# Performance work log

Measured on AMD Instinct MI355X. Metric: run time of the kernel, lower is better.

Reference implementation:

```python
import jax, jax.numpy as jnp
import numpy as np


def setup_inputs() -> dict:
    key = jax.random.key(0)
    k1, k2 = jax.random.split(key)
    embeddings = jax.random.normal(k1, (32, 512, 1024), dtype=jnp.float32)
    aspect = jax.random.normal(k2, (32, 1024), dtype=jnp.float32)
    return {"embeddings": embeddings, "aspect": aspect}


def reference(embeddings, aspect):
    # go_backwards=False, so no sequence reversal.
    # L2-normalize embeddings per token and aspect per sample.
    e = embeddings / jnp.linalg.norm(embeddings, axis=2, keepdims=True)
    a = aspect / jnp.linalg.norm(aspect, axis=1, keepdims=True)
    # NaN-mask (zero-norm rows produce NaN after division).
    e = jnp.where(jnp.isnan(e), jnp.zeros_like(e), e)
    a = jnp.where(jnp.isnan(a), jnp.zeros_like(a), a)
    # Circulant matrix: circ[b, i, j] = a[b, (j - i) mod D]
    # (matches the TF scatter_nd construction M[i, (i+k)%D] = a[k]).
    D = e.shape[-1]
    r = jnp.arange(D)
    idx = (r[None, :] - r[:, None]) % D  # [D, D]
    circ = a[:, idx]  # [B, D, D]
    # matmul(e, circ, transpose_b=True): out[b,s,i] = sum_j e[b,s,j] * circ[b,i,j]
    return jnp.einsum('bsd,bid->bsi', e, circ)
```

## Files before the change

kernel.cpp:

```cpp
#include <hip/hip_runtime.h>
#include <hip/hip_bf16.h>

typedef __attribute__((ext_vector_type(8))) short bf16x8;
typedef __attribute__((ext_vector_type(4))) float f32x4;

#define NB 32
#define NS 512
#define ND 1024

__device__ __forceinline__ unsigned short f2bf(float f) {
  unsigned int u = __float_as_uint(f);
  u = (u + 0x7FFFu + ((u >> 16) & 1u)) >> 16;
  return (unsigned short)u;
}

__global__ void anorm_kernel(const float* __restrict__ aspect,
                             unsigned short* __restrict__ a_n) {
  int b = blockIdx.x;
  int t = threadIdx.x;
  const float4* p = (const float4*)(aspect + (size_t)b * ND);
  float4 v = p[t];
  float s = v.x * v.x + v.y * v.y + v.z * v.z + v.w * v.w;
#pragma unroll
  for (int off = 32; off >= 1; off >>= 1) s += __shfl_down(s, off);
  __shared__ float red[4];
  if ((t & 63) == 0) red[t >> 6] = s;
  __syncthreads();
  float tot = red[0] + red[1] + red[2] + red[3];
  float inv = (tot > 0.f) ? (1.f / sqrtf(tot)) : 0.f;
  ushort4 u;
  u.x = f2bf(v.x * inv); u.y = f2bf(v.y * inv);
  u.z = f2bf(v.z * inv); u.w = f2bf(v.w * inv);
  ((ushort4*)(a_n + (size_t)b * ND))[t] = u;
}

__global__ __launch_bounds__(256)
void enormbf_kernel(const float* __restrict__ emb,
                    unsigned short* __restrict__ eN) {
  int wave = threadIdx.x >> 6, lane = threadIdx.x & 63;
  size_t row = (size_t)blockIdx.x * 4 + wave;
  const float4* p = (const float4*)(emb + row * ND);
  float4 v[4];
  float s = 0.f;
#pragma unroll
  for (int j = 0; j < 4; ++j) {
    v[j] = p[lane + 64 * j];
    s += v[j].x * v[j].x + v[j].y * v[j].y + v[j].z * v[j].z + v[j].w * v[j].w;
  }
#pragma unroll
  for (int off = 32; off >= 1; off >>= 1) s += __shfl_xor(s, off);
  float inv = (s > 0.f) ? (1.f / sqrtf(s)) : 0.f;
  ushort4* o = (ushort4*)(eN + row * ND);
#pragma unroll
  for (int j = 0; j < 4; ++j) {
    ushort4 u;
    u.x = f2bf(v[j].x * inv); u.y = f2bf(v[j].y * inv);
    u.z = f2bf(v[j].z * inv); u.w = f2bf(v[j].w * inv);
    o[lane + 64 * j] = u;
  }
}

__global__ __launch_bounds__(256, 4)
void corr_gemm3_kernel(const unsigned short* __restrict__ eN,
                       const unsigned short* __restrict__ a_n,
                       float* __restrict__ out) {
  __shared__ unsigned short copies[8][1160];
  __shared__ unsigned short Atile[128 * 64];

  const int b = blockIdx.x, mt = blockIdx.y, nt = blockIdx.z;
  const int n0 = nt * 128, m0 = mt * 128;
  const int t = threadIdx.x;

  {
    const unsigned short* an = a_n + (size_t)b * ND;
    int p = t & 7;
    int x0 = (t >> 3) * 36;
    int base = (896 - n0 + p) & 1023;
#pragma unroll
    for (int j = 0; j < 36; j += 4) {
      ushort4 u;
      u.x = an[(base + x0 + j + 0) & 1023];
      u.y = an[(base + x0 + j + 1) & 1023];
      u.z = an[(base + x0 + j + 2) & 1023];
      u.w = an[(base + x0 + j + 3) & 1023];
      *(ushort4*)&copies[p][x0 + j] = u;
    }
  }

  const int lane = t & 63, wv = t >> 6;
  const int wm = wv >> 1, wn = wv & 1;
  const int q = lane >> 4, l16 = lane & 15;

  const int srow = wv * 8 + (lane >> 3);
  const int sc = (lane & 7) ^ (lane >> 3);
  const unsigned short* gsrc = eN + ((size_t)b * NS + m0 + srow) * ND + sc * 8;
  char* ldsA = (char*)Atile;
  const int ldst0 = wv * 1024 + lane * 16;

  f32x4 acc[4][4];
#pragma unroll
  for (int i = 0; i < 4; ++i)
#pragma unroll
    for (int j = 0; j < 4; ++j)
      acc[i][j] = (f32x4){0.f, 0.f, 0.f, 0.f};

  for (int k0 = 0; k0 < ND; k0 += 64) {
    __syncthreads();
#pragma unroll
    for (int j = 0; j < 4; ++j) {
      __builtin_amdgcn_global_load_lds(
          (const __attribute__((address_space(1))) void*)(gsrc + (size_t)j * 32 * ND + k0),
          (__attribute__((address_space(3))) void*)(ldsA + ldst0 + j * 4096),
          16, 0, 0);
    }
    __syncthreads();

#pragma unroll
    for (int kk = 0; kk < 2; ++kk) {
      bf16x8 af[4], bfr[4];
#pragma unroll
      for (int r = 0; r < 4; ++r) {
        int m = wm * 64 + r * 16 + l16;
        int c = kk * 4 + q;
        int s = c ^ (m & 7);
        af[r] = *(const bf16x8*)&Atile[m * 64 + s * 8];

        int idx = k0 + kk * 32 + 8 * q + 128 - (wn * 64 + r * 16 + l16);
        int p = idx & 7;
        bfr[r] = *(const bf16x8*)&copies[p][idx - p];
      }
#pragma unroll
      for (int i = 0; i < 4; ++i)
#pragma unroll
        for (int j2 = 0; j2 < 4; ++j2)
          acc[i][j2] = __builtin_amdgcn_mfma_f32_16x16x32_bf16(af[i], bfr[j2], acc[i][j2], 0, 0, 0);
    }
  }

  float* outB = out + ((size_t)b * NS + m0) * ND + n0;
#pragma unroll
  for (int i = 0; i < 4; ++i) {
#pragma unroll
    for (int rg = 0; rg < 4; ++rg) {
      int s = wm * 64 + i * 16 + q * 4 + rg;
      float* orow = outB + (size_t)s * ND + wn * 64 + l16;
#pragma unroll
      for (int j = 0; j < 4; ++j)
        orow[j * 16] = acc[i][j][rg];
    }
  }
}

__global__ void enorm_kernel(const float* __restrict__ emb,
                             float* __restrict__ inv_norm) {
  int wave = threadIdx.x >> 6;
  int lane = threadIdx.x & 63;
  int row = blockIdx.x * 4 + wave;
  const float4* p = (const float4*)(emb + (size_t)row * ND);
  float s = 0.f;
#pragma unroll
  for (int j = 0; j < 4; ++j) {
    float4 v = p[lane + 64 * j];
    s += v.x * v.x + v.y * v.y + v.z * v.z + v.w * v.w;
  }
#pragma unroll
  for (int off = 32; off >= 1; off >>= 1) s += __shfl_down(s, off);
  if (lane == 0) inv_norm[row] = (s > 0.f) ? (1.f / sqrtf(s)) : 0.f;
}

__global__ __launch_bounds__(256)
void corr_gemm_kernel(const float* __restrict__ emb,
                      const float* __restrict__ inv_norm,
                      const unsigned short* __restrict__ a_n,
                      float* __restrict__ out) {
  __shared__ unsigned short copies[8][2056];
  __shared__ unsigned short Atile[128][40];

  const int nt = blockIdx.x, mt = blockIdx.y, b = blockIdx.z;
  const int n0 = nt * 128, m0 = mt * 128;
  const int t = threadIdx.x;

  {
    const unsigned short* an = a_n + (size_t)b * ND;
    int p = t & 7;
    int x0 = (t >> 3) * 64;
#pragma unroll
    for (int j = 0; j < 64; j += 4) {
      ushort4 u;
      u.x = an[(x0 + j + 0 + p) & 1023];
      u.y = an[(x0 + j + 1 + p) & 1023];
      u.z = an[(x0 + j + 2 + p) & 1023];
      u.w = an[(x0 + j + 3 + p) & 1023];
      *(ushort4*)&copies[p][x0 + j] = u;
    }
  }

  const int ar = t >> 3;
  const int ac = (t & 7) * 4;
  float invn[4];
#pragma unroll
  for (int w = 0; w < 4; ++w)
    invn[w] = inv_norm[b * NS + m0 + ar + 32 * w];

  const int lane = t & 63;
  const int wv = t >> 6;
  const int wm = wv >> 1, wn = wv & 1;
  const int q = lane >> 4, l16 = lane & 15;

  f32x4 acc[4][4];
#pragma unroll
  for (int i = 0; i < 4; ++i)
#pragma unroll
    for (int j = 0; j < 4; ++j)
      acc[i][j] = (f32x4){0.f, 0.f, 0.f, 0.f};

  const float* embB = emb + ((size_t)b * NS + m0) * ND;

  for (int k0 = 0; k0 < ND; k0 += 32) {
    __syncthreads();
#pragma unroll
    for (int w = 0; w < 4; ++w) {
      int r = ar + 32 * w;
      float4 v = *(const float4*)(embB + (size_t)r * ND + k0 + ac);
      float in = invn[w];
      ushort4 u;
      u.x = f2bf(v.x * in); u.y = f2bf(v.y * in);
      u.z = f2bf(v.z * in); u.w = f2bf(v.w * in);
      *(ushort4*)&Atile[r][ac] = u;
    }
    __syncthreads();

    bf16x8 af[4], bfr[4];
#pragma unroll
    for (int r = 0; r < 4; ++r) {
      int m = wm * 64 + r * 16 + l16;
      af[r] = *(const bf16x8*)&Atile[m][q * 8];
    }
#pragma unroll
    for (int r = 0; r < 4; ++r) {
      int ng = n0 + wn * 64 + r * 16 + l16;
      int e0 = k0 + 8 * q - ng + 1024;
      int p = e0 & 7;
      bfr[r] = *(const bf16x8*)&copies[p][e0 - p];
    }
#pragma unroll
    for (int i = 0; i < 4; ++i)
#pragma unroll
      for (int j = 0; j < 4; ++j)
        acc[i][j] = __builtin_amdgcn_mfma_f32_16x16x32_bf16(af[i], bfr[j], acc[i][j], 0, 0, 0);
  }

  float* outB = out + ((size_t)b * NS + m0) * ND + n0;
#pragma unroll
  for (int i = 0; i < 4; ++i) {
#pragma unroll
    for (int rg = 0; rg < 4; ++rg) {
      int s = wm * 64 + i * 16 + q * 4 + rg;
      float* orow = outB + (size_t)s * ND + wn * 64 + l16;
#pragma unroll
      for (int j = 0; j < 4; ++j)
        orow[j * 16] = acc[i][j][rg];
    }
  }
}

extern "C" void kernel_launch(void* const* d_in, const int* in_sizes, int n_in,
                              void* d_out, int out_size, void* d_ws, size_t ws_size,
                              hipStream_t stream) {
  const float* emb = (const float*)d_in[0];
  const float* aspect = (const float*)d_in[1];
  float* out = (float*)d_out;

  const size_t need = 65536 + (size_t)NB * NS * ND * 2;

  if (ws_size >= need) {
    unsigned short* a_n = (unsigned short*)d_ws;
    unsigned short* eN = (unsigned short*)((char*)d_ws + 65536);
    anorm_kernel<<<NB, 256, 0, stream>>>(aspect, a_n);
    enormbf_kernel<<<4096, 256, 0, stream>>>(emb, eN);
    corr_gemm3_kernel<<<dim3(NB, 4, 8), 256, 0, stream>>>(eN, a_n, out);
  } else {
    float* inv_norm = (float*)d_ws;
    unsigned short* a_n = (unsigned short*)((char*)d_ws + 65536);
    enorm_kernel<<<4096, 256, 0, stream>>>(emb, inv_norm);
    anorm_kernel<<<NB, 256, 0, stream>>>(aspect, a_n);
    corr_gemm_kernel<<<dim3(8, 4, NB), 256, 0, stream>>>(emb, inv_norm, a_n, out);
  }
}
```

Before: 144.0 us.

## Use 256x256 tiles with triple-buffered async LDS pipeline in circulant GEMM

Replaces the 128x128, 256-thread GEMM with a 256x256 tile and 512-thread (8-wave) block, so each block does more output work and reuses more data per load. The A tile moves into a three-slot LDS ring. Global-to-LDS loads for stage k+2 are issued inside the compute phases and gated with explicit vmcnt waits and s_barrier instead of full __syncthreads. MFMA bursts are raised with s_setprio, and the circulant B fragments are read from shifted copies with a precomputed base pointer. The goal is to hide memory latency behind MFMA work and cut sync and address overhead. The trade-off is a grid of only 256 blocks with heavy register and LDS use per block, which lowers occupancy.

New measurement: 144.4 us. About the same (+0.3%).

```diff
diff --git a/kernel.cpp b/kernel.cpp
--- a/kernel.cpp
+++ b/kernel.cpp
@@ -60,93 +60,152 @@
   }
 }
 
-__global__ __launch_bounds__(256, 4)
-void corr_gemm3_kernel(const unsigned short* __restrict__ eN,
+__global__ __launch_bounds__(512, 2)
+void corr_gemm4_kernel(const unsigned short* __restrict__ eN,
                        const unsigned short* __restrict__ a_n,
                        float* __restrict__ out) {
-  __shared__ unsigned short copies[8][1160];
-  __shared__ unsigned short Atile[128 * 64];
+  __shared__ __align__(16) unsigned short Alds[3 * 16384];
+  __shared__ __align__(16) unsigned short copies[8 * 1288];
 
   const int b = blockIdx.x, mt = blockIdx.y, nt = blockIdx.z;
-  const int n0 = nt * 128, m0 = mt * 128;
-  const int t = threadIdx.x;
+  const int n0 = nt * 256, m0 = mt * 256;
+  const int tid = threadIdx.x;
 
   {
     const unsigned short* an = a_n + (size_t)b * ND;
-    int p = t & 7;
-    int x0 = (t >> 3) * 36;
-    int base = (896 - n0 + p) & 1023;
-#pragma unroll
-    for (int j = 0; j < 36; j += 4) {
+    const int p = tid & 7;
+    const int x0 = (tid >> 3) * 20;
+    const int base = (768 - n0 + p) & 1023;
+#pragma unroll
+    for (int j = 0; j < 20; j += 4) {
       ushort4 u;
       u.x = an[(base + x0 + j + 0) & 1023];
       u.y = an[(base + x0 + j + 1) & 1023];
       u.z = an[(base + x0 + j + 2) & 1023];
       u.w = an[(base + x0 + j + 3) & 1023];
-      *(ushort4*)&copies[p][x0 + j] = u;
-    }
-  }
-
-  const int lane = t & 63, wv = t >> 6;
-  const int wm = wv >> 1, wn = wv & 1;
+      *(ushort4*)&copies[p * 1288 + x0 + j] = u;
+    }
+  }
+
+  const int lane = tid & 63, wv = tid >> 6;
+  const int wm = wv >> 2, wn = wv & 3;
   const int q = lane >> 4, l16 = lane & 15;
-
-  const int srow = wv * 8 + (lane >> 3);
-  const int sc = (lane & 7) ^ (lane >> 3);
-  const unsigned short* gsrc = eN + ((size_t)b * NS + m0 + srow) * ND + sc * 8;
-  char* ldsA = (char*)Atile;
-  const int ldst0 = wv * 1024 + lane * 16;
-
-  f32x4 acc[4][4];
-#pragma unroll
-  for (int i = 0; i < 4; ++i)
+  const int mx = l16 & 7;
+  const int s00 = (q ^ mx) * 8;
+  const int s01 = ((4 + q) ^ mx) * 8;
+  const int arow = (wm * 128 + l16) * 64;
+
+  const int pB = (8 - mx) & 7;
+  const unsigned short* Bp = copies + pB * 1287 + (256 + 8 * q - wn * 64 - l16);
+
+  const unsigned short* gstage =
+      eN + ((size_t)b * NS + m0 + (tid >> 3)) * ND + (size_t)(((tid & 7) ^ ((tid >> 3) & 7)) * 8);
+  char* ldsAbase = (char*)Alds;
+
+  f32x4 acc[8][4];
+#pragma unroll
+  for (int i = 0; i < 8; ++i)
 #pragma unroll
     for (int j = 0; j < 4; ++j)
       acc[i][j] = (f32x4){0.f, 0.f, 0.f, 0.f};
 
-  for (int k0 = 0; k0 < ND; k0 += 64) {
-    __syncthreads();
-#pragma unroll
-    for (int j = 0; j < 4; ++j) {
-      __builtin_amdgcn_global_load_lds(
-          (const __attribute__((address_space(1))) void*)(gsrc + (size_t)j * 32 * ND + k0),
-          (__attribute__((address_space(3))) void*)(ldsA + ldst0 + j * 4096),
-          16, 0, 0);
-    }
-    __syncthreads();
-
-#pragma unroll
-    for (int kk = 0; kk < 2; ++kk) {
-      bf16x8 af[4], bfr[4];
-#pragma unroll
-      for (int r = 0; r < 4; ++r) {
-        int m = wm * 64 + r * 16 + l16;
-        int c = kk * 4 + q;
-        int s = c ^ (m & 7);
-        af[r] = *(const bf16x8*)&Atile[m * 64 + s * 8];
-
-        int idx = k0 + kk * 32 + 8 * q + 128 - (wn * 64 + r * 16 + l16);
-        int p = idx & 7;
-        bfr[r] = *(const bf16x8*)&copies[p][idx - p];
+  __syncthreads();
+#pragma unroll
+  for (int j = 0; j < 4; ++j)
+    __builtin_amdgcn_global_load_lds(
+        (const __attribute__((address_space(1))) void*)(gstage + (size_t)j * 64 * ND),
+        (__attribute__((address_space(3))) void*)(ldsAbase + (size_t)tid * 16 + j * 8192),
+        16, 0, 0);
+#pragma unroll
+  for (int j = 0; j < 4; ++j)
+    __builtin_amdgcn_global_load_lds(
+        (const __attribute__((address_space(1))) void*)(gstage + (size_t)j * 64 * ND + 64),
+        (__attribute__((address_space(3))) void*)(ldsAbase + 32768 + (size_t)tid * 16 + j * 8192),
+        16, 0, 0);
+  asm volatile("s_waitcnt vmcnt(4)" ::: "memory");
+  __builtin_amdgcn_sched_barrier(0);
+  __builtin_amdgcn_s_barrier();
+
+  int c0 = 0, c1 = 1, c2 = 2;
+
+#define STAGE_PAIR(J0)                                                                   \
+  do {                                                                                   \
+    if (kt + 2 < 16) {                                                                   \
+      const unsigned short* sg_ = gstage + (size_t)(kt + 2) * 64;                        \
+      char* dl_ = ldsAbase + c2 * 32768 + (size_t)tid * 16;                              \
+      __builtin_amdgcn_global_load_lds(                                                  \
+          (const __attribute__((address_space(1))) void*)(sg_ + (size_t)(J0) * 64 * ND), \
+          (__attribute__((address_space(3))) void*)(dl_ + (J0) * 8192), 16, 0, 0);       \
+      __builtin_amdgcn_global_load_lds(                                                  \
+          (const __attribute__((address_space(1))) void*)(sg_ + (size_t)((J0) + 1) * 64 * ND), \
+          (__attribute__((address_space(3))) void*)(dl_ + ((J0) + 1) * 8192), 16, 0, 0); \
+    }                                                                                    \
+  } while (0)
+
+#define GEMM_PHASE(PH, EXTRA)                                                            \
+  do {                                                                                   \
+    bf16x8 aA0  = *(const bf16x8*)&At[arow + (PH)*2048 + s00];                           \
+    bf16x8 aA0k = *(const bf16x8*)&At[arow + (PH)*2048 + s01];                           \
+    bf16x8 aA1  = *(const bf16x8*)&At[arow + (PH)*2048 + 1024 + s00];                    \
+    bf16x8 aA1k = *(const bf16x8*)&At[arow + (PH)*2048 + 1024 + s01];                    \
+    EXTRA;                                                                               \
+    __builtin_amdgcn_s_barrier();                                                        \
+    asm volatile("s_waitcnt lgkmcnt(0)" ::: "memory");                                   \
+    __builtin_amdgcn_sched_barrier(0);                                                   \
+    __builtin_amdgcn_s_setprio(1);                                                       \
+    _Pragma("unroll")                                                                    \
+    for (int n = 0; n < 4; ++n) {                                                        \
+      acc[2*(PH)][n]   = __builtin_amdgcn_mfma_f32_16x16x32_bf16(aA0,  bfr[n][0], acc[2*(PH)][n],   0, 0, 0); \
+      acc[2*(PH)][n]   = __builtin_amdgcn_mfma_f32_16x16x32_bf16(aA0k, bfr[n][1], acc[2*(PH)][n],   0, 0, 0); \
+      acc[2*(PH)+1][n] = __builtin_amdgcn_mfma_f32_16x16x32_bf16(aA1,  bfr[n][0], acc[2*(PH)+1][n], 0, 0, 0); \
+      acc[2*(PH)+1][n] = __builtin_amdgcn_mfma_f32_16x16x32_bf16(aA1k, bfr[n][1], acc[2*(PH)+1][n], 0, 0, 0); \
+    }                                                                                    \
+    __builtin_amdgcn_s_setprio(0);                                                       \
+  } while (0)
+
+#pragma unroll 1
+  for (int kt = 0; kt < 16; ++kt) {
+    const unsigned short* At = Alds + c0 * 16384;
+
+    bf16x8 bfr[4][2];
+    {
+      const unsigned short* Bt = Bp + kt * 64;
+#pragma unroll
+      for (int n = 0; n < 4; ++n) {
+        bfr[n][0] = *(const bf16x8*)(Bt - n * 16);
+        bfr[n][1] = *(const bf16x8*)(Bt + 32 - n * 16);
       }
-#pragma unroll
-      for (int i = 0; i < 4; ++i)
-#pragma unroll
-        for (int j2 = 0; j2 < 4; ++j2)
-          acc[i][j2] = __builtin_amdgcn_mfma_f32_16x16x32_bf16(af[i], bfr[j2], acc[i][j2], 0, 0, 0);
-    }
-  }
+    }
+    GEMM_PHASE(0, STAGE_PAIR(0));
+    __builtin_amdgcn_s_barrier();
+    GEMM_PHASE(1, STAGE_PAIR(2));
+    __builtin_amdgcn_s_barrier();
+    GEMM_PHASE(2, );
+    __builtin_amdgcn_s_barrier();
+    GEMM_PHASE(3, );
+    if (kt < 14) {
+      asm volatile("s_waitcnt vmcnt(4)" ::: "memory");
+    } else if (kt == 14) {
+      asm volatile("s_waitcnt vmcnt(0)" ::: "memory");
+    }
+    __builtin_amdgcn_sched_barrier(0);
+    __builtin_amdgcn_s_barrier();
+
+    int tmp = c0; c0 = c1; c1 = c2; c2 = tmp;
+  }
+#undef GEMM_PHASE
+#undef STAGE_PAIR
 
   float* outB = out + ((size_t)b * NS + m0) * ND + n0;
 #pragma unroll
-  for (int i = 0; i < 4; ++i) {
+  for (int i = 0; i < 8; ++i) {
 #pragma unroll
     for (int rg = 0; rg < 4; ++rg) {
-      int s = wm * 64 + i * 16 + q * 4 + rg;
-      float* orow = outB + (size_t)s * ND + wn * 64 + l16;
-#pragma unroll
-      for (int j = 0; j < 4; ++j)
-        orow[j * 16] = acc[i][j][rg];
+      int r = wm * 128 + i * 16 + q * 4 + rg;
+      float* orow = outB + (size_t)r * ND + wn * 64 + l16;
+#pragma unroll
+      for (int n = 0; n < 4; ++n)
+        orow[n * 16] = acc[i][n][rg];
     }
   }
 }
@@ -278,7 +337,7 @@
     unsigned short* eN = (unsigned short*)((char*)d_ws + 65536);
     anorm_kernel<<<NB, 256, 0, stream>>>(aspect, a_n);
     enormbf_kernel<<<4096, 256, 0, stream>>>(emb, eN);
-    corr_gemm3_kernel<<<dim3(NB, 4, 8), 256, 0, stream>>>(eN, a_n, out);
+    corr_gemm4_kernel<<<dim3(NB, 2, 4), 512, 0, stream>>>(eN, a_n, out);
   } else {
     float* inv_norm = (float*)d_ws;
     unsigned short* a_n = (unsigned short*)((char*)d_ws + 65536);
```
